# Optimization experiments

Hardware: AMD Instinct MI355X
Metric: run time of the kernel (lower is better)

The kernel has to match this reference:

```python
import jax, jax.numpy as jnp
import numpy as np

LEAKY_SLOPE = 0.2

def setup_inputs() -> dict:
    key = jax.random.key(0)
    k1, k2, k3, k4, k5 = jax.random.split(key, 5)
    N, F_IN, H, D = 8192, 256, 4, 64
    x = jax.random.normal(k1, (N, F_IN), dtype=jnp.float32)
    adj = jax.random.randint(k2, (N, N), 0, 2, dtype=jnp.int32)
    W = jax.random.normal(k3, (F_IN, H * D), dtype=jnp.float32) * 0.05
    a_l = jax.random.normal(k4, (H, D), dtype=jnp.float32) * 0.05
    a_r = jax.random.normal(k5, (H, D), dtype=jnp.float32) * 0.05
    return {"x": x, "adj": adj, "W": W, "a_l": a_l, "a_r": a_r}

def reference(x, adj, W, a_l, a_r):
    N = x.shape[0]
    H, D = a_l.shape
    # projected node features: (N, H, D)
    h = (x @ W).reshape(N, H, D)
    score_l = jnp.einsum('nhd,hd->nh', h, a_l)  # (N, H)
    score_r = jnp.einsum('nhd,hd->nh', h, a_r)  # (N, H)
    # logits[i, j, h] = score_l[i, h] + score_r[j, h]
    logits = score_l[:, None, :] + score_r[None, :, :]
    logits = jax.nn.leaky_relu(logits, negative_slope=LEAKY_SLOPE)
    # mask: keep edge (i,j) if adj[i,j] + eye[i,j] != 0
    keep = (adj + jnp.eye(N, dtype=adj.dtype)) != 0  # (N, N)
    logits = jnp.where(keep[:, :, None], logits, -jnp.inf)
    # softmax over neighbors j (axis=1), matching torch softmax(dim=1)
    attn = jax.nn.softmax(logits, axis=1)  # (N, N, H)
    out = jnp.einsum('ijh,jhf->ihf', attn, h)  # (N, H, D)
    return out.reshape(N, H * D)  # concat=True
```

## Files before the change

kernel.cpp:

```cpp
#include <hip/hip_runtime.h>
#include <hip/hip_bf16.h>

#define N 8192
#define FIN 256
#define HD 256
#define LEAKY 0.2f

typedef short sh8 __attribute__((ext_vector_type(8)));
typedef float f32x4 __attribute__((ext_vector_type(4)));
typedef int   i32x4 __attribute__((ext_vector_type(4)));

__device__ __forceinline__ int pack2bf(float a, float b){
  __hip_bfloat162 t = __float22bfloat162_rn(make_float2(a, b));
  union { __hip_bfloat162 h; int i; } u;
  u.h = t;
  return u.i;
}

__device__ __forceinline__ unsigned bf16hi_rne(float v){
  unsigned u = __float_as_uint(v);
  u += 0x7FFFu + ((u >> 16) & 1u);
  return u >> 16;
}

__global__ void k_wt(const float* __restrict__ W, __hip_bfloat16* __restrict__ Wt){
  __shared__ float t[16][17];
  int tx = threadIdx.x, ty = threadIdx.y;
  int bx = blockIdx.x*16, by = blockIdx.y*16;
  t[ty][tx] = W[(by+ty)*HD + (bx+tx)];
  __syncthreads();
  Wt[(bx+ty)*FIN + (by+tx)] = __float2bfloat16(t[tx][ty]);
}

__global__ __launch_bounds__(256, 2) void k_h(
    const float* __restrict__ x, const __hip_bfloat16* __restrict__ Wt,
    const float* __restrict__ a_l, const float* __restrict__ a_r,
    __hip_bfloat16* __restrict__ ht, float* __restrict__ El, float* __restrict__ El2,
    unsigned* __restrict__ ee)
{
  const int lane = threadIdx.x & 63;
  const int w = threadIdx.x >> 6;
  const int r0 = lane & 15, q = lane >> 4;
  const int c0 = w*64;
  const int n0 = blockIdx.x*32;

  f32x4 acc[4][2];
  #pragma unroll
  for (int m = 0; m < 4; ++m)
    #pragma unroll
    for (int nt = 0; nt < 2; ++nt)
      acc[m][nt] = (f32x4){0.f, 0.f, 0.f, 0.f};

  for (int kb = 0; kb < 8; ++kb){
    const int k = kb*32 + q*8;
    sh8 af[4];
    #pragma unroll
    for (int m = 0; m < 4; ++m)
      af[m] = *(const sh8*)(Wt + (c0 + m*16 + r0)*FIN + k);
    #pragma unroll
    for (int nt = 0; nt < 2; ++nt){
      const float* xp = x + (n0 + nt*16 + r0)*FIN + k;
      f32x4 xl = *(const f32x4*)xp;
      f32x4 xh = *(const f32x4*)(xp + 4);
      union { sh8 s; int i[4]; } bx;
      bx.i[0] = pack2bf(xl[0], xl[1]);
      bx.i[1] = pack2bf(xl[2], xl[3]);
      bx.i[2] = pack2bf(xh[0], xh[1]);
      bx.i[3] = pack2bf(xh[2], xh[3]);
      #pragma unroll
      for (int m = 0; m < 4; ++m)
        acc[m][nt] = __builtin_amdgcn_mfma_f32_16x16x32_bf16(af[m], bx.s, acc[m][nt], 0, 0, 0);
    }
  }

  float pl[2] = {0.f, 0.f}, pr[2] = {0.f, 0.f};
  #pragma unroll
  for (int m = 0; m < 4; ++m){
    #pragma unroll
    for (int reg = 0; reg < 4; ++reg){
      const int c = c0 + m*16 + q*4 + reg;
      const float alv = a_l[c], arv = a_r[c];
      #pragma unroll
      for (int nt = 0; nt < 2; ++nt){
        float v = acc[m][nt][reg];
        ht[(size_t)c*N + (n0 + nt*16 + r0)] = __float2bfloat16(v);
        pl[nt] += v*alv;
        pr[nt] += v*arv;
      }
    }
  }
  #pragma unroll
  for (int nt = 0; nt < 2; ++nt){
    pl[nt] += __shfl_xor(pl[nt], 16); pl[nt] += __shfl_xor(pl[nt], 32);
    pr[nt] += __shfl_xor(pr[nt], 16); pr[nt] += __shfl_xor(pr[nt], 32);
  }
  if (lane < 16){
    #pragma unroll
    for (int nt = 0; nt < 2; ++nt){
      const int n = n0 + nt*16 + r0;
      const float l = pl[nt], r = pr[nt];
      El [w*N + n] = __expf(l);
      El2[w*N + n] = __expf(LEAKY*l);
      float er  = __expf(r);
      float er2 = __expf(LEAKY*r);
      ee[w*N + n] = bf16hi_rne(er) | (bf16hi_rne(er2) << 16);
    }
  }
}

__global__ __launch_bounds__(256) void k_bits(const int* __restrict__ adj,
                                              unsigned long long* __restrict__ bits)
{
  const int lane = threadIdx.x & 63;
  const int wid = (blockIdx.x*256 + threadIdx.x) >> 6;
  const int nw = (gridDim.x*256) >> 6;
  const int total = (N/64)*N;
  for (int idx = wid; idx < total; idx += nw){
    const int r = idx >> 7, c = idx & 127;
    int av = __builtin_nontemporal_load(adj + (size_t)r*N + c*64 + lane);
    unsigned long long b = __ballot(av != 0);
    if (c == (r >> 6)) b |= 1ull << (r & 63);
    if (lane == 0) bits[idx] = b;
  }
}

__device__ __forceinline__ void sub_compute(
    const sh8 hf[4], const i32x4 ee2[2], unsigned swm0, unsigned swm1,
    const float el[2], const float el2[2], int q, const sh8& ones,
    f32x4 acc[2][4], f32x4 accz[2])
{
  float er[8], er2[8];
  #pragma unroll
  for (int e = 0; e < 8; ++e){
    unsigned u = (e < 4) ? (unsigned)ee2[0][e] : (unsigned)ee2[1][e-4];
    er[e]  = __uint_as_float(u << 16);
    er2[e] = __uint_as_float(u & 0xFFFF0000u);
  }
  #pragma unroll
  for (int m = 0; m < 2; ++m){
    const unsigned sw = ((m == 0) ? swm0 : swm1) >> (q*8);
    unsigned fi[4];
    #pragma unroll
    for (int p = 0; p < 4; ++p){
      float w0 = fmaxf(el[m]*er[2*p],   el2[m]*er2[2*p]);
      float w1 = fmaxf(el[m]*er[2*p+1], el2[m]*er2[2*p+1]);
      w0 = (sw & (1u << (2*p)))   ? w0 : 0.0f;
      w1 = (sw & (1u << (2*p+1))) ? w1 : 0.0f;
      fi[p] = __builtin_amdgcn_perm(__float_as_uint(w1), __float_as_uint(w0), 0x07060302u);
    }
    union { sh8 s; unsigned u[4]; } fa;
    fa.u[0]=fi[0]; fa.u[1]=fi[1]; fa.u[2]=fi[2]; fa.u[3]=fi[3];
    #pragma unroll
    for (int d = 0; d < 4; ++d)
      acc[m][d] = __builtin_amdgcn_mfma_f32_16x16x32_bf16(fa.s, hf[d], acc[m][d], 0, 0, 0);
    accz[m] = __builtin_amdgcn_mfma_f32_16x16x32_bf16(fa.s, ones, accz[m], 0, 0, 0);
  }
}

__global__ __launch_bounds__(256, 4) void k_attn(
    const unsigned* __restrict__ bits32, const __hip_bfloat16* __restrict__ ht,
    const float* __restrict__ El, const float* __restrict__ El2,
    const unsigned* __restrict__ ee, float* __restrict__ part, float* __restrict__ zpart)
{
  __shared__ __align__(16) char smem[32768];
  const int b = blockIdx.x;
  const int h = b & 3, jq = (b >> 2) & 3, i128 = b >> 4;
  const int tid = threadIdx.x;
  const int lane = tid & 63;
  const int w = tid >> 6;
  const int r0 = lane & 15, q = lane >> 4;
  const int ib = i128*128 + w*32;
  const int jbase = jq * 2048;

  const __hip_bfloat16* gp = ht + (size_t)(h*64 + w*16 + (lane >> 2))*N
                                + jbase + (lane & 3)*8;
  char* lb = smem + w*1024;

  const char* frp = smem + r0*64 + q*16;

  const float* el_ = El  + h*N + ib + r0;
  const float* el2_= El2 + h*N + ib + r0;
  const float el[2]  = { el_[0],  el_[16]  };
  const float el2[2] = { el2_[0], el2_[16] };
  const unsigned* bp0 = bits32 + (size_t)(ib + r0)*(N/32) + (jbase >> 5);
  const unsigned* bp1 = bp0 + 16*(N/32);
  const unsigned* eeq = ee + h*N + jbase + q*8;

  union { sh8 s; int i[4]; } onef;
  {
    int v = (r0 == 0) ? 0x3F803F80 : 0;
    onef.i[0]=v; onef.i[1]=v; onef.i[2]=v; onef.i[3]=v;
  }

  f32x4 acc[2][4];
  f32x4 accz[2];
  #pragma unroll
  for (int m = 0; m < 2; ++m){
    accz[m] = (f32x4){0.f,0.f,0.f,0.f};
    #pragma unroll
    for (int d = 0; d < 4; ++d)
      acc[m][d] = (f32x4){0.f,0.f,0.f,0.f};
  }

#define STAGE(bufoff, t) do { \
    const __hip_bfloat16* _g = gp + (t)*128; \
    _Pragma("unroll") \
    for (int _s = 0; _s < 4; ++_s) \
      __builtin_amdgcn_global_load_lds( \
        (const __attribute__((address_space(1))) void*)(_g + _s*32), \
        (__attribute__((address_space(3))) void*)(lb + (bufoff) + _s*4096), 16, 0, 0); \
  } while(0)

#define LD_HF(dst, bufoff, ss) do { \
    _Pragma("unroll") \
    for (int _d = 0; _d < 4; ++_d) \
      dst[_d] = *(const sh8*)(frp + (bufoff) + (ss)*4096 + _d*1024); \
  } while(0)

#define LD_EE(dst, t, ss) do { \
    dst[0] = *(const i32x4*)(eeq + (t)*128 + (ss)*32); \
    dst[1] = *(const i32x4*)(eeq + (t)*128 + (ss)*32 + 4); \
  } while(0)

  sh8   hfc[4], hfn[4];
  i32x4 eec[2], een[2];
  i32x4 bw0, bw1;

  STAGE(0, 0);
  __syncthreads();
  LD_HF(hfc, 0, 0);
  LD_EE(eec, 0, 0);
  bw0 = *(const i32x4*)(bp0);
  bw1 = *(const i32x4*)(bp1);

  for (int t = 0; t < 16; ++t){
    const int bo = (t & 1) ? 16384 : 0;
    const int bn = bo ^ 16384;
    const int tn = (t+1 < 16) ? t+1 : 0;
    STAGE(bn, tn);

    #pragma unroll
    for (int ss = 0; ss < 3; ++ss){
      LD_HF(hfn, bo, ss+1);
      LD_EE(een, t, ss+1);
      sub_compute(hfc, eec, (unsigned)bw0[ss], (unsigned)bw1[ss],
                  el, el2, q, onef.s, acc, accz);
      #pragma unroll
      for (int d = 0; d < 4; ++d) hfc[d] = hfn[d];
      eec[0] = een[0]; eec[1] = een[1];
    }
    i32x4 nb0 = *(const i32x4*)(bp0 + tn*4);
    i32x4 nb1 = *(const i32x4*)(bp1 + tn*4);
    sub_compute(hfc, eec, (unsigned)bw0[3], (unsigned)bw1[3],
                el, el2, q, onef.s, acc, accz);
    __syncthreads();
    LD_HF(hfc, bn, 0);
    LD_EE(eec, tn, 0);
    bw0 = nb0; bw1 = nb1;
  }

  if (r0 == 0){
    #pragma unroll
    for (int m = 0; m < 2; ++m)
      #pragma unroll
      for (int reg = 0; reg < 4; ++reg)
        zpart[(jq*4 + h)*N + ib + m*16 + q*4 + reg] = accz[m][reg];
  }

  float* pp = part + (size_t)jq*N*HD + h*64 + r0;
  #pragma unroll
  for (int m = 0; m < 2; ++m)
    #pragma unroll
    for (int d = 0; d < 4; ++d)
      #pragma unroll
      for (int reg = 0; reg < 4; ++reg)
        pp[(size_t)(ib + m*16 + q*4 + reg)*HD + d*16] = acc[m][d][reg];
#undef STAGE
#undef LD_HF
#undef LD_EE
}

__global__ void k_out(const float* __restrict__ part, const float* __restrict__ zpart,
                      float* __restrict__ out)
{
  const int t4 = (blockIdx.x*256 + threadIdx.x) * 4;
  const int i = t4 >> 8;
  const int h = (t4 & 255) >> 6;
  f32x4 a = *(const f32x4*)(part + t4);
  f32x4 bq = *(const f32x4*)(part + (size_t)N*HD + t4);
  f32x4 c = *(const f32x4*)(part + 2*(size_t)N*HD + t4);
  f32x4 d = *(const f32x4*)(part + 3*(size_t)N*HD + t4);
  float zz = zpart[h*N + i] + zpart[(4 + h)*N + i] + zpart[(8 + h)*N + i] + zpart[(12 + h)*N + i];
  f32x4 s = (a + bq + c + d) / zz;
  *(f32x4*)(out + t4) = s;
}

extern "C" void kernel_launch(void* const* d_in, const int* in_sizes, int n_in,
                              void* d_out, int out_size, void* d_ws, size_t ws_size,
                              hipStream_t stream) {
  const float* x   = (const float*)d_in[0];
  const int*   adj = (const int*)d_in[1];
  const float* W   = (const float*)d_in[2];
  const float* a_l = (const float*)d_in[3];
  const float* a_r = (const float*)d_in[4];
  float* out = (float*)d_out;

  char* ws = (char*)d_ws;
  __hip_bfloat16* Wt = (__hip_bfloat16*)ws;
  __hip_bfloat16* ht = (__hip_bfloat16*)(ws + 131072);
  float*    El   = (float*)   (ws + 4325376);
  float*    El2  = (float*)   (ws + 4456448);
  unsigned* ee   = (unsigned*)(ws + 4587520);
  unsigned long long* bits = (unsigned long long*)(ws + 4718592);
  float*    part = (float*)   (ws + 13107200);
  float*    zpart= (float*)   (ws + 46661632);

  k_wt  <<<dim3(16,16), dim3(16,16), 0, stream>>>(W, Wt);
  k_h   <<<256, 256, 0, stream>>>(x, Wt, a_l, a_r, ht, El, El2, ee);
  k_bits<<<4096, 256, 0, stream>>>(adj, bits);
  k_attn<<<1024, 256, 0, stream>>>((const unsigned*)bits, ht, El, El2, ee, part, zpart);
  k_out <<<N*HD/1024, 256, 0, stream>>>(part, zpart, out);
}
```

Measured before the change: 486.2 us.

## Switch attention weights to packed fp16 math with swizzled LDS layout

```diff
diff --git a/kernel.cpp b/kernel.cpp
--- a/kernel.cpp
+++ b/kernel.cpp
@@ -1,5 +1,6 @@
 #include <hip/hip_runtime.h>
 #include <hip/hip_bf16.h>
+#include <hip/hip_fp16.h>
 
 #define N 8192
 #define FIN 256
@@ -7,6 +8,8 @@
 #define LEAKY 0.2f
 
 typedef short sh8 __attribute__((ext_vector_type(8)));
+typedef _Float16 h8 __attribute__((ext_vector_type(8)));
+typedef _Float16 h2 __attribute__((ext_vector_type(2)));
 typedef float f32x4 __attribute__((ext_vector_type(4)));
 typedef int   i32x4 __attribute__((ext_vector_type(4)));
 
@@ -17,11 +20,8 @@
   return u.i;
 }
 
-__device__ __forceinline__ unsigned bf16hi_rne(float v){
-  unsigned u = __float_as_uint(v);
-  u += 0x7FFFu + ((u >> 16) & 1u);
-  return u >> 16;
-}
+__device__ __forceinline__ h2 u2h2(unsigned u){ union{unsigned u; h2 h;} c; c.u=u; return c.h; }
+__device__ __forceinline__ unsigned h22u(h2 h){ union{unsigned u; h2 h;} c; c.h=h; return c.u; }
 
 __global__ void k_wt(const float* __restrict__ W, __hip_bfloat16* __restrict__ Wt){
   __shared__ float t[16][17];
@@ -35,8 +35,8 @@
 __global__ __launch_bounds__(256, 2) void k_h(
     const float* __restrict__ x, const __hip_bfloat16* __restrict__ Wt,
     const float* __restrict__ a_l, const float* __restrict__ a_r,
-    __hip_bfloat16* __restrict__ ht, float* __restrict__ El, float* __restrict__ El2,
-    unsigned* __restrict__ ee)
+    _Float16* __restrict__ ht, float* __restrict__ El, float* __restrict__ El2,
+    _Float16* __restrict__ Erh, _Float16* __restrict__ Er2h)
 {
   const int lane = threadIdx.x & 63;
   const int w = threadIdx.x >> 6;
@@ -83,7 +83,7 @@
       #pragma unroll
       for (int nt = 0; nt < 2; ++nt){
         float v = acc[m][nt][reg];
-        ht[(size_t)c*N + (n0 + nt*16 + r0)] = __float2bfloat16(v);
+        ht[(size_t)c*N + (n0 + nt*16 + r0)] = (_Float16)v;
         pl[nt] += v*alv;
         pr[nt] += v*arv;
       }
@@ -99,11 +99,10 @@
     for (int nt = 0; nt < 2; ++nt){
       const int n = n0 + nt*16 + r0;
       const float l = pl[nt], r = pr[nt];
-      El [w*N + n] = __expf(l);
-      El2[w*N + n] = __expf(LEAKY*l);
-      float er  = __expf(r);
-      float er2 = __expf(LEAKY*r);
-      ee[w*N + n] = bf16hi_rne(er) | (bf16hi_rne(er2) << 16);
+      El  [w*N + n] = __expf(l);
+      El2 [w*N + n] = __expf(LEAKY*l);
+      Erh [w*N + n] = (_Float16)__expf(r);
+      Er2h[w*N + n] = (_Float16)__expf(LEAKY*r);
     }
   }
 }
@@ -125,42 +124,46 @@
 }
 
 __device__ __forceinline__ void sub_compute(
-    const sh8 hf[4], const i32x4 ee2[2], unsigned swm0, unsigned swm1,
-    const float el[2], const float el2[2], int q, const sh8& ones,
-    f32x4 acc[2][4], f32x4 accz[2])
-{
-  float er[8], er2[8];
-  #pragma unroll
-  for (int e = 0; e < 8; ++e){
-    unsigned u = (e < 4) ? (unsigned)ee2[0][e] : (unsigned)ee2[1][e-4];
-    er[e]  = __uint_as_float(u << 16);
-    er2[e] = __uint_as_float(u & 0xFFFF0000u);
-  }
+    const char* frp, int loff, const _Float16* erq, const _Float16* er2q, int eoff,
+    unsigned sw0, unsigned sw1, const h2 elh[2], const h2 el2h[2], int q,
+    const h8& ones, f32x4 acc[2][4], f32x4 accz[2])
+{
+  h8 hf[4];
+  #pragma unroll
+  for (int d = 0; d < 4; ++d)
+    hf[d] = *(const h8*)(frp + loff + d*1024);
+
+  i32x4 er4  = *(const i32x4*)(erq  + eoff);
+  i32x4 er24 = *(const i32x4*)(er2q + eoff);
+
   #pragma unroll
   for (int m = 0; m < 2; ++m){
-    const unsigned sw = ((m == 0) ? swm0 : swm1) >> (q*8);
-    unsigned fi[4];
+    const unsigned sw = ((m == 0) ? sw0 : sw1) >> (q*8);
+    unsigned fu[4];
     #pragma unroll
     for (int p = 0; p < 4; ++p){
-      float w0 = fmaxf(el[m]*er[2*p],   el2[m]*er2[2*p]);
-      float w1 = fmaxf(el[m]*er[2*p+1], el2[m]*er2[2*p+1]);
-      w0 = (sw & (1u << (2*p)))   ? w0 : 0.0f;
-      w1 = (sw & (1u << (2*p+1))) ? w1 : 0.0f;
-      fi[p] = __builtin_amdgcn_perm(__float_as_uint(w1), __float_as_uint(w0), 0x07060302u);
+      h2 w2 = __builtin_elementwise_max(elh[m]  * u2h2((unsigned)er4[p]),
+                                        el2h[m] * u2h2((unsigned)er24[p]));
+      unsigned wu = h22u(w2);
+      const unsigned t = sw >> (2*p);
+      wu = (t & 1u) ? wu : (wu & 0xFFFF0000u);
+      wu = (t & 2u) ? wu : (wu & 0x0000FFFFu);
+      fu[p] = wu;
     }
-    union { sh8 s; unsigned u[4]; } fa;
-    fa.u[0]=fi[0]; fa.u[1]=fi[1]; fa.u[2]=fi[2]; fa.u[3]=fi[3];
+    union { h8 s; unsigned u[4]; } fa;
+    fa.u[0]=fu[0]; fa.u[1]=fu[1]; fa.u[2]=fu[2]; fa.u[3]=fu[3];
     #pragma unroll
     for (int d = 0; d < 4; ++d)
-      acc[m][d] = __builtin_amdgcn_mfma_f32_16x16x32_bf16(fa.s, hf[d], acc[m][d], 0, 0, 0);
-    accz[m] = __builtin_amdgcn_mfma_f32_16x16x32_bf16(fa.s, ones, accz[m], 0, 0, 0);
+      acc[m][d] = __builtin_amdgcn_mfma_f32_16x16x32_f16(fa.s, hf[d], acc[m][d], 0, 0, 0);
+    accz[m] = __builtin_amdgcn_mfma_f32_16x16x32_f16(fa.s, ones, accz[m], 0, 0, 0);
   }
 }
 
 __global__ __launch_bounds__(256, 4) void k_attn(
-    const unsigned* __restrict__ bits32, const __hip_bfloat16* __restrict__ ht,
+    const unsigned* __restrict__ bits32, const _Float16* __restrict__ ht,
     const float* __restrict__ El, const float* __restrict__ El2,
-    const unsigned* __restrict__ ee, float* __restrict__ part, float* __restrict__ zpart)
+    const _Float16* __restrict__ Erh, const _Float16* __restrict__ Er2h,
+    float* __restrict__ part, float* __restrict__ zpart)
 {
   __shared__ __align__(16) char smem[32768];
   const int b = blockIdx.x;
@@ -172,23 +175,30 @@
   const int ib = i128*128 + w*32;
   const int jbase = jq * 2048;
 
-  const __hip_bfloat16* gp = ht + (size_t)(h*64 + w*16 + (lane >> 2))*N
-                                + jbase + (lane & 3)*8;
+  const _Float16* gp = ht + (size_t)(h*64 + w*16 + (lane >> 2))*N
+                          + jbase + (((lane & 3) ^ ((lane >> 3) & 3))*8);
   char* lb = smem + w*1024;
 
-  const char* frp = smem + r0*64 + q*16;
+  const char* frp = smem + r0*64 + ((q ^ ((r0 >> 1) & 3)) << 4);
 
   const float* el_ = El  + h*N + ib + r0;
   const float* el2_= El2 + h*N + ib + r0;
-  const float el[2]  = { el_[0],  el_[16]  };
-  const float el2[2] = { el2_[0], el2_[16] };
+  h2 elh[2], el2h[2];
+  #pragma unroll
+  for (int m = 0; m < 2; ++m){
+    _Float16 a = (_Float16)el_[m*16];
+    _Float16 c = (_Float16)el2_[m*16];
+    elh[m]  = (h2){a, a};
+    el2h[m] = (h2){c, c};
+  }
   const unsigned* bp0 = bits32 + (size_t)(ib + r0)*(N/32) + (jbase >> 5);
   const unsigned* bp1 = bp0 + 16*(N/32);
-  const unsigned* eeq = ee + h*N + jbase + q*8;
-
-  union { sh8 s; int i[4]; } onef;
+  const _Float16* erq  = Erh  + h*N + jbase + q*8;
+  const _Float16* er2q = Er2h + h*N + jbase + q*8;
+
+  union { h8 s; int i[4]; } onef;
   {
-    int v = (r0 == 0) ? 0x3F803F80 : 0;
+    int v = (r0 == 0) ? 0x3C003C00 : 0;
     onef.i[0]=v; onef.i[1]=v; onef.i[2]=v; onef.i[3]=v;
   }
 
@@ -203,7 +213,7 @@
   }
 
 #define STAGE(bufoff, t) do { \
-    const __hip_bfloat16* _g = gp + (t)*128; \
+    const _Float16* _g = gp + (t)*128; \
     _Pragma("unroll") \
     for (int _s = 0; _s < 4; ++_s) \
       __builtin_amdgcn_global_load_lds( \
@@ -211,52 +221,24 @@
         (__attribute__((address_space(3))) void*)(lb + (bufoff) + _s*4096), 16, 0, 0); \
   } while(0)
 
-#define LD_HF(dst, bufoff, ss) do { \
-    _Pragma("unroll") \
-    for (int _d = 0; _d < 4; ++_d) \
-      dst[_d] = *(const sh8*)(frp + (bufoff) + (ss)*4096 + _d*1024); \
-  } while(0)
-
-#define LD_EE(dst, t, ss) do { \
-    dst[0] = *(const i32x4*)(eeq + (t)*128 + (ss)*32); \
-    dst[1] = *(const i32x4*)(eeq + (t)*128 + (ss)*32 + 4); \
-  } while(0)
-
-  sh8   hfc[4], hfn[4];
-  i32x4 eec[2], een[2];
-  i32x4 bw0, bw1;
-
   STAGE(0, 0);
   __syncthreads();
-  LD_HF(hfc, 0, 0);
-  LD_EE(eec, 0, 0);
-  bw0 = *(const i32x4*)(bp0);
-  bw1 = *(const i32x4*)(bp1);
 
   for (int t = 0; t < 16; ++t){
     const int bo = (t & 1) ? 16384 : 0;
     const int bn = bo ^ 16384;
-    const int tn = (t+1 < 16) ? t+1 : 0;
+    const int tn = (t + 1) & 15;
     STAGE(bn, tn);
 
-    #pragma unroll
-    for (int ss = 0; ss < 3; ++ss){
-      LD_HF(hfn, bo, ss+1);
-      LD_EE(een, t, ss+1);
-      sub_compute(hfc, eec, (unsigned)bw0[ss], (unsigned)bw1[ss],
-                  el, el2, q, onef.s, acc, accz);
-      #pragma unroll
-      for (int d = 0; d < 4; ++d) hfc[d] = hfn[d];
-      eec[0] = een[0]; eec[1] = een[1];
-    }
-    i32x4 nb0 = *(const i32x4*)(bp0 + tn*4);
-    i32x4 nb1 = *(const i32x4*)(bp1 + tn*4);
-    sub_compute(hfc, eec, (unsigned)bw0[3], (unsigned)bw1[3],
-                el, el2, q, onef.s, acc, accz);
+    i32x4 bw0 = *(const i32x4*)(bp0 + t*4);
+    i32x4 bw1 = *(const i32x4*)(bp1 + t*4);
+    #pragma unroll
+    for (int ss = 0; ss < 4; ++ss)
+      sub_compute(frp, bo + ss*4096, erq, er2q, t*128 + ss*32,
+                  (unsigned)bw0[ss], (unsigned)bw1[ss],
+                  elh, el2h, q, onef.s, acc, accz);
+
     __syncthreads();
-    LD_HF(hfc, bn, 0);
-    LD_EE(eec, tn, 0);
-    bw0 = nb0; bw1 = nb1;
   }
 
   if (r0 == 0){
@@ -276,8 +258,6 @@
       for (int reg = 0; reg < 4; ++reg)
         pp[(size_t)(ib + m*16 + q*4 + reg)*HD + d*16] = acc[m][d][reg];
 #undef STAGE
-#undef LD_HF
-#undef LD_EE
 }
 
 __global__ void k_out(const float* __restrict__ part, const float* __restrict__ zpart,
@@ -307,17 +287,18 @@
 
   char* ws = (char*)d_ws;
   __hip_bfloat16* Wt = (__hip_bfloat16*)ws;
-  __hip_bfloat16* ht = (__hip_bfloat16*)(ws + 131072);
+  _Float16* ht   = (_Float16*)(ws + 131072);
   float*    El   = (float*)   (ws + 4325376);
   float*    El2  = (float*)   (ws + 4456448);
-  unsigned* ee   = (unsigned*)(ws + 4587520);
+  _Float16* Erh  = (_Float16*)(ws + 4587520);
+  _Float16* Er2h = (_Float16*)(ws + 4653056);
   unsigned long long* bits = (unsigned long long*)(ws + 4718592);
   float*    part = (float*)   (ws + 13107200);
   float*    zpart= (float*)   (ws + 46661632);
 
   k_wt  <<<dim3(16,16), dim3(16,16), 0, stream>>>(W, Wt);
-  k_h   <<<256, 256, 0, stream>>>(x, Wt, a_l, a_r, ht, El, El2, ee);
+  k_h   <<<256, 256, 0, stream>>>(x, Wt, a_l, a_r, ht, El, El2, Erh, Er2h);
   k_bits<<<4096, 256, 0, stream>>>(adj, bits);
-  k_attn<<<1024, 256, 0, stream>>>((const unsigned*)bits, ht, El, El2, ee, part, zpart);
+  k_attn<<<1024, 256, 0, stream>>>((const unsigned*)bits, ht, El, El2, Erh, Er2h, part, zpart);
   k_out <<<N*HD/1024, 256, 0, stream>>>(part, zpart, out);
 }
```

New measurement: 485.9 us. About the same (-0.1%).
